# Performance work log

Measured on AMD Instinct MI355X. Metric: run time of the kernel, lower is better.

The kernel has to match this reference:

```python
import jax, jax.numpy as jnp
import numpy as np

B, K, C = 8192, 64, 8  # batch, feature dim, number of private-attribute classes


def setup_inputs() -> dict:
    key = jax.random.key(0)
    k1, k2, k3 = jax.random.split(key, 3)
    mu = jax.random.normal(k1, (B, K), dtype=jnp.float32)
    private_attribute = jax.random.randint(k2, (B,), 0, C)
    A = jax.random.normal(k3, (K, K), dtype=jnp.float32) * 0.05
    cov = A @ A.T + jnp.eye(K, dtype=jnp.float32)  # SPD prior covariance
    return {"mu": mu, "private_attribute": private_attribute, "cov": cov}


def _kldiv(mu1, S1, mu2, S2, k):
    # KL( N(mu1,S1) || N(mu2,S2) )
    d = mu2 - mu1
    tr = jnp.trace(jnp.linalg.solve(S2, S1))       # tr(inv(S2) S1)
    quad = d @ jnp.linalg.solve(S2, d)             # d^T inv(S2) d
    ld2 = jnp.linalg.slogdet(S2)[1]
    ld1 = jnp.linalg.slogdet(S1)[1]
    return 0.5 * (tr + quad - k + ld2 - ld1)


def reference(mu, private_attribute, cov):
    Bn, k = mu.shape
    labels = private_attribute
    ones = jnp.ones((Bn,), mu.dtype)
    counts = jax.ops.segment_sum(ones, labels, num_segments=C)                # [C]
    safe = jnp.maximum(counts, 1.0)
    mu_F = jax.ops.segment_sum(mu, labels, num_segments=C) / safe[:, None]    # [C,k] group means
    mu_total = jnp.mean(mu, axis=0)                                           # [k]
    dt = mu - mu_total
    Sigma_total = cov + dt.T @ dt / Bn                                        # [k,k]
    dc = mu - mu_F[labels]                                                    # [B,k]
    outer = jnp.einsum('bi,bj->bij', dc, dc)                                  # [B,k,k]
    Sigma_F = cov + jax.ops.segment_sum(outer, labels, num_segments=C) / safe[:, None, None]  # [C,k,k]
    kl = jax.vmap(lambda m, S: _kldiv(m, S, mu_total, Sigma_total, k))(mu_F, Sigma_F)  # [C]
    # The original loops `for i in range(len(keys)-1)` over dict keys ordered by
    # first occurrence in the batch, i.e. it SKIPS the class whose first sample
    # appears latest. Reproduce that exactly.
    pos = jnp.arange(Bn)
    first_pos = jnp.min(
        jnp.where(labels[:, None] == jnp.arange(C)[None, :], pos[:, None], Bn), axis=0
    )                                                                          # [C]
    present = first_pos < Bn
    last_key = jnp.argmax(jnp.where(present, first_pos, -1))
    w = jnp.where(present & (jnp.arange(C) != last_key), counts, 0.0)          # count_Fs weights
    result = jnp.sum(kl * w * Bn) / (Bn ** 2)
    return result
```

## Files before the change

### kernel.cpp

```cpp
#include <hip/hip_runtime.h>

#define CC 8
#define KK 64
#define BB 8192
#define NCHUNK 16
#define NGBLK (NCHUNK * CC)
#define ROWS_PER_CHUNK (BB / NCHUNK)

#define OFF_G     0
#define OFF_GSUM  262144
#define OFF_GCNT  264192
#define OFF_CNTR  264224
#define OFF_FLG   264228
#define OFF_GFST  264232
#define OFF_INV   264264
#define OFF_LD2   297032
#define OFF_TERMS 297040

#define SM_BUFA  0
#define SM_BUFB  4160
#define SM_PANEL 8320
#define SM_LB    8832
#define SM_LDI   12992
#define SM_MB    13056
#define SM_INTS  13120
#define SMEM_BACK 13128

__device__ __forceinline__ double readlane_f64(double v, int lane) {
  union { double d; int i[2]; } u, r;
  u.d = v;
  r.i[0] = __builtin_amdgcn_readlane(u.i[0], lane);
  r.i[1] = __builtin_amdgcn_readlane(u.i[1], lane);
  return r.d;
}

__global__ __launch_bounds__(256) void k_front(const float* __restrict__ mu,
                                               const int* __restrict__ labels, char* ws) {
  __shared__ double smem[2176];
  int blk = blockIdx.x;
  int chunk = blk >> 3, c = blk & 7;
  int tid = threadIdx.x;
  int lane = tid & 63, w = tid >> 6;
  int tx = tid & 15, ty = tid >> 4;
  float* rows = (float*)smem;
  int* labs = (int*)(smem + 2048);
  float* ssum = (float*)(smem + 2080);
  int* scnt = (int*)(smem + 2112);
  int* sfst = (int*)(smem + 2114);
  double* G = (double*)(ws + OFF_G);
  float* gsum = (float*)(ws + OFF_GSUM);
  int* gcount = (int*)(ws + OFF_GCNT);
  int* gfirst = (int*)(ws + OFF_GFST);

  double acc[4][4] = {{0.0}};
  float rsum = 0.f;
  int cnt = 0, first = BB;
  int base = chunk * ROWS_PER_CHUNK;
  const float4* mu4 = (const float4*)mu + (size_t)base * (KK / 4);
  if (tid < KK) ssum[tid] = 0.f;

  float4 pf[4];
  int plab = 0;
#pragma unroll
  for (int i = 0; i < 4; ++i) pf[i] = mu4[tid + i * 256];
  if (tid < 64) plab = labels[base + tid];

#pragma unroll 1
  for (int g = 0; g < ROWS_PER_CHUNK / 64; ++g) {
    __syncthreads();
    float4* rows4 = (float4*)rows;
#pragma unroll
    for (int i = 0; i < 4; ++i) rows4[tid + i * 256] = pf[i];
    if (tid < 64) labs[tid] = plab;
    __syncthreads();
    if (g + 1 < ROWS_PER_CHUNK / 64) {
#pragma unroll
      for (int i = 0; i < 4; ++i) pf[i] = mu4[(g + 1) * 1024 + tid + i * 256];
      if (tid < 64) plab = labels[base + (g + 1) * 64 + tid];
    }
#pragma unroll 4
    for (int r = 0; r < 16; ++r) {
      int rr = w * 16 + r;
      if (labs[rr] == c) rsum += rows[rr * KK + lane];
    }
    if (lane < 16 && labs[w * 16 + lane] == c) {
      cnt++;
      first = min(first, base + g * 64 + w * 16 + lane);
    }
    unsigned long long m = __ballot(labs[lane] == c);
    while (m) {
      int r = __builtin_ctzll(m);
      m &= m - 1;
      const float4* rw4 = (const float4*)(rows + r * KK);
      float4 a4 = rw4[ty], b4 = rw4[tx];
      const float* ai = (const float*)&a4;
      const float* bj = (const float*)&b4;
#pragma unroll
      for (int a = 0; a < 4; ++a)
#pragma unroll
        for (int b = 0; b < 4; ++b) acc[a][b] += (double)ai[a] * (double)bj[b];
    }
  }
  double* Gc = G + (size_t)c * KK * KK;
#pragma unroll
  for (int a = 0; a < 4; ++a)
#pragma unroll
    for (int b = 0; b < 4; ++b)
      atomicAdd(&Gc[(ty * 4 + a) * KK + tx * 4 + b], acc[a][b]);
  atomicAdd(&ssum[lane], rsum);
#pragma unroll
  for (int off = 32; off; off >>= 1) {
    cnt += __shfl_down(cnt, off);
    first = min(first, __shfl_down(first, off));
  }
  if (lane == 0) { scnt[w] = cnt; sfst[w] = first; }
  __syncthreads();
  if (tid < KK) {
    float v = ssum[tid];
    if (v != 0.f) atomicAdd(&gsum[c * KK + tid], v);
  }
  if (tid == 0) {
    int ct = scnt[0] + scnt[1] + scnt[2] + scnt[3];
    if (ct) {
      atomicAdd(&gcount[c], ct);
      atomicMin(&gfirst[c], min(min(sfst[0], sfst[1]), min(sfst[2], sfst[3])));
    }
  }
}

__device__ __noinline__ double chol64(double* smem, bool isS2) {
  int tid = threadIdx.x;
  int t = tid & 63, w = tid >> 6;
  double (*bufA)[KK + 1] = (double (*)[KK + 1])(smem + SM_BUFA);
  double (*bufB)[KK + 1] = (double (*)[KK + 1])(smem + SM_BUFB);
  double (*panelb)[KK] = (double (*)[KK])(smem + SM_PANEL);
  double (*Lb)[KK + 1] = (double (*)[KK + 1])(smem + SM_LB);
  double* Ldi = smem + SM_LDI;
  double (*cur)[KK + 1] = bufA;
  double (*nxt)[KK + 1] = bufB;
  double ldacc = 0.0;
  int bound = t | 7;
#pragma unroll 1
  for (int p = 0; p < 8; ++p) {
    const int P0 = p * 8;
    double cc_[8];
#pragma unroll
    for (int m = 0; m < 8; ++m) cc_[m] = cur[t][P0 + m];
    double uu[8];
    double pd = 1.0;
#pragma unroll
    for (int m = 0; m < 8; ++m) {
      double akk = readlane_f64(cc_[m], P0 + m);
      pd *= akk;
      double inv;
      asm("v_rcp_f64 %0, %1" : "=v"(inv) : "v"(akk));
      inv = inv * fma(-akk, inv, 2.0);
      uu[m] = cc_[m] * inv;
      if (w == 0) {
        panelb[m][t] = cc_[m];
        if (isS2) {
          double rsv = sqrt(akk) * inv;
          Lb[t][P0 + m] = cc_[m] * rsv;
          if (t == 0) Ldi[P0 + m] = rsv;
        }
      }
#pragma unroll
      for (int mm = m + 1; mm < 8; ++mm)
        cc_[mm] -= uu[m] * readlane_f64(cc_[m], P0 + mm);
    }
    ldacc += log(pd);
    __syncthreads();
#pragma unroll 1
    for (int jb = p + 1 + w; jb < 8; jb += 4) {
      int j = jb * 8;
      if (j <= bound) {
        double aj[8];
#pragma unroll
        for (int q = 0; q < 8; ++q) aj[q] = cur[t][j + q];
#pragma unroll
        for (int m = 0; m < 8; ++m)
#pragma unroll
          for (int q = 0; q < 8; ++q) aj[q] -= uu[m] * panelb[m][j + q];
#pragma unroll
        for (int q = 0; q < 8; ++q) nxt[t][j + q] = aj[q];
      }
    }
    __syncthreads();
    { auto tmp = cur; cur = nxt; nxt = tmp; }
  }
  return ldacc;
}

__global__ __launch_bounds__(256) void k_back(const float* __restrict__ cov,
                                              float* out, char* ws) {
  __shared__ double smem[SMEM_BACK];
  int blk = blockIdx.x;
  int tid = threadIdx.x;
  int t = tid & 63, w = tid >> 6;
  double* G = (double*)(ws + OFF_G);
  float* gsum = (float*)(ws + OFF_GSUM);
  int* gcount = (int*)(ws + OFF_GCNT);
  int* gfirst = (int*)(ws + OFF_GFST);
  double* invS2 = (double*)(ws + OFF_INV);
  double* ld2g = (double*)(ws + OFF_LD2);
  double* terms = (double*)(ws + OFF_TERMS);
  int* cntr = (int*)(ws + OFF_CNTR);
  int* flg = (int*)(ws + OFF_FLG);
  double* mb = smem + SM_MB;
  int* cnt8s = (int*)(smem + SM_INTS);
  int* fst8s = cnt8s + 8;

  if (blk < CC) {
    int c = blk;
    if (tid < 64) {
      double st = 0.0;
#pragma unroll
      for (int cc2 = 0; cc2 < CC; ++cc2) st += (double)gsum[cc2 * KK + t];
      smem[SM_LDI + t] = st * (1.0 / (double)BB);
      smem[SM_MB + t] = (double)gsum[c * KK + t];
    } else if (tid < 80) {
      int j = tid - 64;
      if (j < 8) cnt8s[j] = gcount[j];
      else fst8s[j - 8] = gfirst[j - 8];
    }
    __syncthreads();
    int nc = cnt8s[c];
    double ncd = (double)nc;
    double safe = nc > 0 ? ncd : 1.0;
    double inv_safe = 1.0 / safe;
    if (tid < 64) {
      double m = smem[SM_MB + t] * inv_safe;
      smem[SM_MB + t] = m;
      smem[SM_LDI + t] -= m;
    }
    __syncthreads();

    double* stash = smem + SM_LB;
    const double* Gc = G + (size_t)c * KK * KK;
#pragma unroll
    for (int q = 0; q < 16; ++q) {
      int e = tid + q * 256;
      int r = e >> 6, c0 = e & 63;
      double v = (double)cov[e] + (Gc[e] - ncd * mb[r] * mb[c0]) * inv_safe;
      smem[SM_BUFA + r * (KK + 1) + c0] = v;
      stash[r * (KK + 1) + c0] = v;
    }
    __syncthreads();

    double ld1 = chol64(smem, false);

    if (tid == 0) {
      int it = 0;
      while (__hip_atomic_load(flg, __ATOMIC_ACQUIRE, __HIP_MEMORY_SCOPE_AGENT) == 0 &&
             ++it < (1 << 20))
        __builtin_amdgcn_s_sleep(8);
    }
    __syncthreads();
    double ld2 = __hip_atomic_load(ld2g, __ATOMIC_RELAXED, __HIP_MEMORY_SCOPE_AGENT);
    double* dvv = smem + SM_LDI;
    double trp = 0.0, qp = 0.0;
#pragma unroll 4
    for (int rr = 0; rr < 16; ++rr) {
      int r = w * 16 + rr;
      double iv = __hip_atomic_load(&invS2[r * KK + t], __ATOMIC_RELAXED,
                                    __HIP_MEMORY_SCOPE_AGENT);
      trp += iv * stash[r * (KK + 1) + t];
      qp += iv * dvv[r];
    }
    qp *= dvv[t];
#pragma unroll
    for (int m = 32; m; m >>= 1) {
      trp += __shfl_down(trp, m);
      qp += __shfl_down(qp, m);
    }
    double* wred = smem + SM_PANEL;
    if (t == 0) { wred[w * 2] = trp; wred[w * 2 + 1] = qp; }
    __syncthreads();
    if (tid == 0) {
      double tr = wred[0] + wred[2] + wred[4] + wred[6];
      double quad = wred[1] + wred[3] + wred[5] + wred[7];
      int best = 0;
      long long bv = -2;
      for (int j = 0; j < CC; ++j) {
        long long v = cnt8s[j] > 0 ? (long long)fst8s[j] : -1;
        if (v > bv) { bv = v; best = j; }
      }
      double kl = 0.5 * (tr + quad - (double)KK + ld2 - ld1);
      double wgt = (nc > 0 && c != best) ? ncd : 0.0;
      double term = kl * wgt / (double)BB;
      atomicExch((unsigned long long*)&terms[c],
                 (unsigned long long)__double_as_longlong(term));
      __threadfence();
      int old = atomicAdd(cntr, 1);
      if (old == CC - 1) {
        double s = 0.0;
        for (int j = 0; j < CC; ++j) s += atomicAdd(&terms[j], 0.0);
        out[0] = (float)s;
      }
    }
  } else {
    if (tid < 64) {
      double st = 0.0;
#pragma unroll
      for (int cc2 = 0; cc2 < CC; ++cc2) st += (double)gsum[cc2 * KK + t];
      mb[t] = st * (1.0 / (double)BB);
    }
    __syncthreads();
    const double invB = 1.0 / (double)BB;
#pragma unroll 1
    for (int q = 0; q < 16; ++q) {
      int e = tid + q * 256;
      double g = 0.0;
#pragma unroll
      for (int c2 = 0; c2 < CC; ++c2) g += G[(size_t)c2 * KK * KK + e];
      int r = e >> 6, c0 = e & 63;
      smem[SM_BUFA + r * (KK + 1) + c0] = (double)cov[e] + g * invB - mb[r] * mb[c0];
    }
    __syncthreads();
    double ld2 = chol64(smem, true);
    double (*Xs)[KK] = (double (*)[KK])(smem + SM_BUFA);
    if (w == 0) {
      double (*Lb)[KK + 1] = (double (*)[KK + 1])(smem + SM_LB);
      double* Ldi = smem + SM_LDI;
#pragma unroll 1
      for (int g = 0; g < 8; ++g) {
        int I0 = g * 8;
        double sv[8];
#pragma unroll
        for (int m = 0; m < 8; ++m) sv[m] = 0.0;
#pragma unroll 2
        for (int j = 0; j < I0; ++j) {
          double xj = Xs[j][t];
#pragma unroll
          for (int m = 0; m < 8; ++m) sv[m] += Lb[I0 + m][j] * xj;
        }
#pragma unroll
        for (int m = 0; m < 8; ++m) {
          int i = I0 + m;
          double x = (((i == t) ? 1.0 : 0.0) - sv[m]) * Ldi[i];
#pragma unroll
          for (int mm = m + 1; mm < 8; ++mm) sv[mm] += Lb[I0 + mm][i] * x;
          Xs[i][t] = x;
        }
      }
    }
    __syncthreads();
#pragma unroll 1
    for (int rr = 0; rr < 16; ++rr) {
      int r = w + rr * 4;
      int k0 = r > t ? r : t;
      double s = 0.0;
#pragma unroll 2
      for (int k = k0; k < KK; ++k) s += Xs[k][r] * Xs[k][t];
      __hip_atomic_store(&invS2[r * KK + t], s, __ATOMIC_RELAXED, __HIP_MEMORY_SCOPE_AGENT);
    }
    __syncthreads();
    if (tid == 0) {
      __hip_atomic_store(ld2g, ld2, __ATOMIC_RELAXED, __HIP_MEMORY_SCOPE_AGENT);
      __threadfence();
      __hip_atomic_store(flg, 1, __ATOMIC_RELEASE, __HIP_MEMORY_SCOPE_AGENT);
    }
  }
}

extern "C" void kernel_launch(void* const* d_in, const int* in_sizes, int n_in,
                              void* d_out, int out_size, void* d_ws, size_t ws_size,
                              hipStream_t stream) {
  (void)in_sizes; (void)n_in; (void)out_size; (void)ws_size;
  const float* mu = (const float*)d_in[0];
  const int* labels = (const int*)d_in[1];
  const float* cov = (const float*)d_in[2];
  float* out = (float*)d_out;
  char* ws = (char*)d_ws;

  hipMemsetAsync(ws, 0, OFF_GFST, stream);
  hipMemsetAsync(ws + OFF_GFST, 0x7f, CC * sizeof(int), stream);

  k_front<<<NGBLK, 256, 0, stream>>>(mu, labels, ws);
  k_back<<<CC + 1, 256, 0, stream>>>(cov, out, ws);
}
```

Baseline: 129.6 us.

## Cholesky update in place via lane broadcasts; spread triangular inverse across waves

The blocked Cholesky now updates a single shared-memory buffer in place. It broadcasts panel values between lanes with readlane instead of staging a panel in LDS and ping-ponging two buffers, which removes one barrier per panel step. The triangular inverse solve splits each group's dot-product accumulation across all four waves, reducing partial sums through shared memory, where only wave 0 did this before. The inverse Gram product now keeps Xs columns in registers and broadcasts them with readlane. It also runs the full k range instead of the triangular start, so it relies on Xs being exactly zero above the diagonal. The register arrays indexed in non-unrolled loops may spill to scratch.

```diff
diff --git a/kernel.cpp b/kernel.cpp
--- a/kernel.cpp
+++ b/kernel.cpp
@@ -18,7 +18,7 @@
 #define OFF_TERMS 297040
 
 #define SM_BUFA  0
-#define SM_BUFB  4160
+#define SM_SPART 4160
 #define SM_PANEL 8320
 #define SM_LB    8832
 #define SM_LDI   12992
@@ -131,13 +131,9 @@
 __device__ __noinline__ double chol64(double* smem, bool isS2) {
   int tid = threadIdx.x;
   int t = tid & 63, w = tid >> 6;
-  double (*bufA)[KK + 1] = (double (*)[KK + 1])(smem + SM_BUFA);
-  double (*bufB)[KK + 1] = (double (*)[KK + 1])(smem + SM_BUFB);
-  double (*panelb)[KK] = (double (*)[KK])(smem + SM_PANEL);
+  double (*A)[KK + 1] = (double (*)[KK + 1])(smem + SM_BUFA);
   double (*Lb)[KK + 1] = (double (*)[KK + 1])(smem + SM_LB);
   double* Ldi = smem + SM_LDI;
-  double (*cur)[KK + 1] = bufA;
-  double (*nxt)[KK + 1] = bufB;
   double ldacc = 0.0;
   int bound = t | 7;
 #pragma unroll 1
@@ -145,7 +141,7 @@
     const int P0 = p * 8;
     double cc_[8];
 #pragma unroll
-    for (int m = 0; m < 8; ++m) cc_[m] = cur[t][P0 + m];
+    for (int m = 0; m < 8; ++m) cc_[m] = A[t][P0 + m];
     double uu[8];
     double pd = 1.0;
 #pragma unroll
@@ -156,37 +152,35 @@
       asm("v_rcp_f64 %0, %1" : "=v"(inv) : "v"(akk));
       inv = inv * fma(-akk, inv, 2.0);
       uu[m] = cc_[m] * inv;
-      if (w == 0) {
-        panelb[m][t] = cc_[m];
-        if (isS2) {
-          double rsv = sqrt(akk) * inv;
-          Lb[t][P0 + m] = cc_[m] * rsv;
-          if (t == 0) Ldi[P0 + m] = rsv;
-        }
+      if (isS2 && w == 0) {
+        double rsv = sqrt(akk) * inv;
+        Lb[t][P0 + m] = cc_[m] * rsv;
+        if (t == 0) Ldi[P0 + m] = rsv;
       }
 #pragma unroll
       for (int mm = m + 1; mm < 8; ++mm)
         cc_[mm] -= uu[m] * readlane_f64(cc_[m], P0 + mm);
     }
     ldacc += log(pd);
-    __syncthreads();
 #pragma unroll 1
     for (int jb = p + 1 + w; jb < 8; jb += 4) {
       int j = jb * 8;
       if (j <= bound) {
         double aj[8];
 #pragma unroll
-        for (int q = 0; q < 8; ++q) aj[q] = cur[t][j + q];
-#pragma unroll
-        for (int m = 0; m < 8; ++m)
-#pragma unroll
-          for (int q = 0; q < 8; ++q) aj[q] -= uu[m] * panelb[m][j + q];
-#pragma unroll
-        for (int q = 0; q < 8; ++q) nxt[t][j + q] = aj[q];
-      }
-    }
-    __syncthreads();
-    { auto tmp = cur; cur = nxt; nxt = tmp; }
+        for (int q = 0; q < 8; ++q) aj[q] = A[t][j + q];
+#pragma unroll
+        for (int m = 0; m < 8; ++m) {
+          double u = uu[m];
+#pragma unroll
+          for (int q = 0; q < 8; ++q)
+            aj[q] -= u * readlane_f64(cc_[m], j + q);
+        }
+#pragma unroll
+        for (int q = 0; q < 8; ++q) A[t][j + q] = aj[q];
+      }
+    }
+    __syncthreads();
   }
   return ldacc;
 }
@@ -319,40 +313,67 @@
     __syncthreads();
     double ld2 = chol64(smem, true);
     double (*Xs)[KK] = (double (*)[KK])(smem + SM_BUFA);
-    if (w == 0) {
-      double (*Lb)[KK + 1] = (double (*)[KK + 1])(smem + SM_LB);
-      double* Ldi = smem + SM_LDI;
-#pragma unroll 1
-      for (int g = 0; g < 8; ++g) {
-        int I0 = g * 8;
-        double sv[8];
-#pragma unroll
-        for (int m = 0; m < 8; ++m) sv[m] = 0.0;
-#pragma unroll 2
-        for (int j = 0; j < I0; ++j) {
-          double xj = Xs[j][t];
-#pragma unroll
-          for (int m = 0; m < 8; ++m) sv[m] += Lb[I0 + m][j] * xj;
-        }
+    double (*Lb)[KK + 1] = (double (*)[KK + 1])(smem + SM_LB);
+    double* Ldi = smem + SM_LDI;
+    double* spart = smem + SM_SPART;
+#pragma unroll 1
+    for (int g = 0; g < 8; ++g) {
+      int I0 = g * 8;
+      double sv[8];
+#pragma unroll
+      for (int m = 0; m < 8; ++m) sv[m] = 0.0;
+#pragma unroll 1
+      for (int j = w; j < I0; j += 4) {
+        double xj = Xs[j][t];
+#pragma unroll
+        for (int m = 0; m < 8; ++m) sv[m] += Lb[I0 + m][j] * xj;
+      }
+#pragma unroll
+      for (int m = 0; m < 8; ++m) spart[(w * 8 + m) * 64 + t] = sv[m];
+      __syncthreads();
+      if (w == 0) {
+        double sv2[8];
+#pragma unroll
+        for (int m = 0; m < 8; ++m)
+          sv2[m] = spart[m * 64 + t] + spart[(8 + m) * 64 + t] +
+                   spart[(16 + m) * 64 + t] + spart[(24 + m) * 64 + t];
 #pragma unroll
         for (int m = 0; m < 8; ++m) {
           int i = I0 + m;
-          double x = (((i == t) ? 1.0 : 0.0) - sv[m]) * Ldi[i];
-#pragma unroll
-          for (int mm = m + 1; mm < 8; ++mm) sv[mm] += Lb[I0 + mm][i] * x;
+          double x = (((i == t) ? 1.0 : 0.0) - sv2[m]) * Ldi[i];
+#pragma unroll
+          for (int mm = m + 1; mm < 8; ++mm) sv2[mm] += Lb[I0 + mm][i] * x;
           Xs[i][t] = x;
         }
       }
-    }
-    __syncthreads();
-#pragma unroll 1
-    for (int rr = 0; rr < 16; ++rr) {
-      int r = w + rr * 4;
-      int k0 = r > t ? r : t;
-      double s = 0.0;
-#pragma unroll 2
-      for (int k = k0; k < KK; ++k) s += Xs[k][r] * Xs[k][t];
-      __hip_atomic_store(&invS2[r * KK + t], s, __ATOMIC_RELAXED, __HIP_MEMORY_SCOPE_AGENT);
+      __syncthreads();
+    }
+    {
+      double s[16];
+#pragma unroll
+      for (int rr = 0; rr < 16; ++rr) s[rr] = 0.0;
+#pragma unroll 1
+      for (int half = 0; half < 2; ++half) {
+        double xt[32];
+        int kb = half * 32;
+#pragma unroll
+        for (int kk = 0; kk < 32; ++kk) xt[kk] = Xs[kb + kk][t];
+#pragma unroll 1
+        for (int rr = 0; rr < 16; ++rr) {
+          int r = w + rr * 4;
+          double acc2 = 0.0;
+#pragma unroll
+          for (int kk = 0; kk < 32; ++kk)
+            acc2 += readlane_f64(xt[kk], r) * xt[kk];
+          s[rr] += acc2;
+        }
+      }
+#pragma unroll 1
+      for (int rr = 0; rr < 16; ++rr) {
+        int r = w + rr * 4;
+        __hip_atomic_store(&invS2[r * KK + t], s[rr], __ATOMIC_RELAXED,
+                           __HIP_MEMORY_SCOPE_AGENT);
+      }
     }
     __syncthreads();
     if (tid == 0) {
```

After: 111.1 us. -14.3%, faster.
